# Optimization experiments

Hardware: AMD Instinct MI355X
Metric: run time of the kernel (lower is better)

## Reference

```python
import jax, jax.numpy as jnp
import numpy as np

B = 8
RESOLUTIONS = [65, 129, 257, 513, 1025]
NUM_POINTS = [0, 4096, 16384, 65536, 262144]
CLIP_MIN = -1e9
FINAL = 1025          # last resolution (both axes)
B_MIN, B_MAX = -1.0, 1.0
BALANCE = 0.5


def setup_inputs() -> dict:
    key = jax.random.key(0)
    k1, k2, k3, k4 = jax.random.split(key, 4)
    return {
        "w1": jax.random.normal(k1, (2, 256), jnp.float32),
        "b1": jax.random.normal(k2, (256,), jnp.float32),
        "w2": jax.random.normal(k3, (256, 1), jnp.float32),
        "b2": jax.random.normal(k4, (1,), jnp.float32),
    }


def _interp_bilinear_ac(x, H, W):
    """F.interpolate(..., mode='bilinear', align_corners=True). x: [B, C, h, w]."""
    b, c, h, w = x.shape
    ys = jnp.linspace(0.0, h - 1.0, H)
    xs = jnp.linspace(0.0, w - 1.0, W)
    y0 = jnp.floor(ys).astype(jnp.int32)
    y1 = jnp.minimum(y0 + 1, h - 1)
    wy = ys - y0
    x0 = jnp.floor(xs).astype(jnp.int32)
    x1 = jnp.minimum(x0 + 1, w - 1)
    wx = xs - x0
    # interpolate rows, then columns
    top = x[:, :, y0, :] * (1.0 - wy)[None, None, :, None] + x[:, :, y1, :] * wy[None, None, :, None]
    return top[:, :, :, x0] * (1.0 - wx) + top[:, :, :, x1] * wx


def _batch_eval(coords, w1, b1, w2, b2):
    """coords: [B, N, 2] in final-resolution pixel space (align_corners=False mapping).
    Returns occupancy [B, N] (C == 1)."""
    coords2d = coords / FINAL + 0.5 / FINAL                 # normalize to [0, 1]
    p = coords2d * (B_MAX - B_MIN) + B_MIN                  # [B, N, 2] in world coords
    h = jax.nn.relu(jnp.einsum('bnd,dh->bnh', p, w1) + b1)  # [B, N, 256]
    occ = jax.nn.sigmoid(jnp.einsum('bnh,ho->bno', h, w2) + b2)
    return occ[..., 0]


def reference(w1, b1, w2, b2):
    occ = None
    for i, res in enumerate(RESOLUTIONS):
        if i == 0:
            # init_coords: grid of res x res points spanning [0, FINAL-1]
            xs = jnp.linspace(0.0, FINAL - 1.0, res)
            gy, gx = jnp.meshgrid(xs, xs, indexing='ij')          # y rows, x cols
            coords = jnp.stack([gx.ravel(), gy.ravel()], axis=-1)  # [N, 2] (x, y)
            coords = jnp.broadcast_to(coords, (B, res * res, 2))
            o = _batch_eval(coords, w1, b1, w2, b2)               # [B, N]
            occ = o.reshape(B, 1, res, res)                       # [B, C, H, W]
        else:
            occ = _interp_bilinear_ac(occ, res, res)
            npt = NUM_POINTS[i]
            if npt <= 0:
                continue
            # uncertainty = -|occ - balance_value|
            unc = -jnp.abs(occ - BALANCE)                          # [B, 1, H, W]
            flat_unc = unc.reshape(B, res * res)
            scores, idx = jax.lax.top_k(flat_unc, npt)             # [B, npt]
            px = (idx % res).astype(jnp.float32)
            py = (idx // res).astype(jnp.float32)
            stride = (FINAL - 1.0) / (res - 1.0)
            coords = jnp.stack([px, py], axis=-1) * stride         # [B, npt, 2]
            new_vals = _batch_eval(coords, w1, b1, w2, b2)         # [B, npt]
            occ_flat = occ.reshape(B, res * res)
            old_vals = jnp.take_along_axis(occ_flat, idx, axis=1)
            vals = jnp.where(scores >= CLIP_MIN, new_vals, old_vals)
            occ_flat = jax.vmap(lambda o, i2, v: o.at[i2].set(v))(occ_flat, idx, vals)
            occ = occ_flat.reshape(B, 1, res, res)
    return occ
```

## Files before the change

kernel.cpp:

```cpp
#include <hip/hip_runtime.h>
#include <stdint.h>

#define HID 256
#define NMAXPIX (1025 * 1025)
#define NREP 4
#define NSEG 2048
#define SELMAX 2112
#define FLAG31 0x80000000u

#define HA_OFF   0
#define HB_OFF   8192
#define HC_OFF   16384
#define SCAL_OFF 20480
#define BLKT_OFF 20544
#define STAGE_U32 21120

#define ALOAD32(p)  __hip_atomic_load((p), __ATOMIC_RELAXED, __HIP_MEMORY_SCOPE_AGENT)
#define ASTORE32(p, v) __hip_atomic_store((p), (v), __ATOMIC_RELAXED, __HIP_MEMORY_SCOPE_AGENT)

__device__ __forceinline__ float mlp_eval4(float wx, float wy,
                                           const float4* __restrict__ w1x,
                                           const float4* __restrict__ w1y,
                                           const float4* __restrict__ vb1,
                                           const float4* __restrict__ vw2, float b2v) {
    const float C0 = (float)(0.5 / 1025.0);
    float px = (wx / 1025.0f + C0) * 2.0f - 1.0f;
    float py = (wy / 1025.0f + C0) * 2.0f - 1.0f;
    float a0 = 0.f, a1 = 0.f, a2 = 0.f, a3 = 0.f;
#pragma unroll 8
    for (int q = 0; q < HID / 4; ++q) {
        float4 a = w1x[q], b = w1y[q], c = vb1[q], d = vw2[q];
        float h0 = px * a.x + py * b.x + c.x;
        float h1 = px * a.y + py * b.y + c.y;
        float h2 = px * a.z + py * b.z + c.z;
        float h3 = px * a.w + py * b.w + c.w;
        h0 = h0 > 0.f ? h0 : 0.f;
        h1 = h1 > 0.f ? h1 : 0.f;
        h2 = h2 > 0.f ? h2 : 0.f;
        h3 = h3 > 0.f ? h3 : 0.f;
        a0 += h0 * d.x;
        a1 += h1 * d.y;
        a2 += h2 * d.z;
        a3 += h3 * d.w;
    }
    float x = ((a0 + a1) + (a2 + a3)) + b2v;
    float r;
    if (x >= 0.f) { r = 1.0f / (1.0f + expf(-x)); }
    else { float e = expf(x); r = e / (1.0f + e); }
    return r;
}

__device__ __forceinline__ uint32_t block_exscan_256(uint32_t v, volatile uint32_t* lds4) {
    int lane = threadIdx.x & 63, w = threadIdx.x >> 6;
    uint32_t inc = v;
#pragma unroll
    for (int d = 1; d < 64; d <<= 1) {
        uint32_t o = (uint32_t)__shfl_up((int)inc, d, 64);
        if (lane >= d) inc += o;
    }
    if (lane == 63) lds4[w] = inc;
    __syncthreads();
    uint32_t woff = 0;
    for (int i = 0; i < w; ++i) woff += lds4[i];
    return woff + inc - v;
}

__device__ void scan_dev(const uint32_t* __restrict__ hist, int NB,
                         uint32_t rem_in, uint32_t prefix_in, int shift,
                         uint32_t* outp, uint32_t* outr,
                         volatile uint32_t* lds4, volatile uint32_t* ldspair) {
    int tid = threadIdx.x;
    int C = NB >> 8;
    int b0 = NB - (tid + 1) * C;
    uint32_t cnts[8];
#pragma unroll
    for (int k = 0; k < 8; ++k) cnts[k] = 0;
    for (int rep = 0; rep < NREP; ++rep) {
        const uint4* p = (const uint4*)(hist + (size_t)rep * NB + b0);
#pragma unroll
        for (int g = 0; g < 2; ++g) {
            if (g * 4 < C) {
                uint4 v = p[g];
                cnts[g * 4 + 0] += v.x;
                cnts[g * 4 + 1] += v.y;
                cnts[g * 4 + 2] += v.z;
                cnts[g * 4 + 3] += v.w;
            }
        }
    }
    uint32_t ssum = 0;
    for (int k = 0; k < C; ++k) ssum += cnts[k];
    uint32_t excl = block_exscan_256(ssum, lds4);
    uint32_t run = excl;
    for (int k = 0; k < C; ++k) {
        uint32_t c = cnts[C - 1 - k];
        if (rem_in > run && rem_in <= run + c) {
            ldspair[0] = (prefix_in << shift) | (uint32_t)(b0 + C - 1 - k);
            ldspair[1] = rem_in - run;
        }
        run += c;
    }
    __syncthreads();
    *outp = ldspair[0];
    *outr = ldspair[1];
}

__global__ __launch_bounds__(256) void k_eval0z(const float* __restrict__ w1, const float* __restrict__ b1,
                                                const float* __restrict__ w2, const float* __restrict__ b2,
                                                float* __restrict__ occ, uint32_t* __restrict__ zbuf, int zcount) {
    __shared__ alignas(16) float sw1[2 * HID];
    __shared__ alignas(16) float sb1[HID];
    __shared__ alignas(16) float sw2[HID];
    int tid = threadIdx.x;
    for (int i = tid; i < 2 * HID; i += 256) sw1[i] = w1[i];
    sb1[tid] = b1[tid];
    sw2[tid] = w2[tid];
    __syncthreads();
    int gtid = blockIdx.x * 256 + tid;
    int nthreads = gridDim.x * 256;
    for (int i = gtid; i < zcount; i += nthreads) zbuf[i] = 0;
    for (int n = gtid; n < 65 * 65; n += nthreads) {
        int i = n / 65, j = n % 65;
        occ[n] = mlp_eval4(16.0f * (float)j, 16.0f * (float)i,
                           (const float4*)sw1, (const float4*)(sw1 + HID),
                           (const float4*)sb1, (const float4*)sw2, b2[0]);
    }
}

__global__ __launch_bounds__(256) void k_upkey(const float* __restrict__ in, int rp,
                                               float* __restrict__ outg, int r, int nb, int bstride,
                                               uint32_t* __restrict__ keys,
                                               uint32_t* __restrict__ histA) {
    __shared__ uint32_t hist[2048];
    int tid = threadIdx.x;
    for (int k = tid; k < 2048; k += 256) hist[k] = 0;
    __syncthreads();
    int N = r * r;
    int lane = tid & 63;
    int gstride = gridDim.x * 256;
    for (int n0 = blockIdx.x * 256; n0 < N; n0 += gstride) {
        int n = n0 + tid;
        bool act = n < N;
        uint32_t key = 0;
        if (act) {
            int i = n / r, j = n % r;
            int i2 = i >> 1, j2 = j >> 1;
            float v;
            if ((i & 1) == 0) {
                if ((j & 1) == 0) {
                    v = in[i2 * rp + j2];
                } else {
                    float a = in[i2 * rp + j2], b = in[i2 * rp + j2 + 1];
                    v = a * 0.5f + b * 0.5f;
                }
            } else {
                if ((j & 1) == 0) {
                    float a = in[i2 * rp + j2], b = in[(i2 + 1) * rp + j2];
                    v = a * 0.5f + b * 0.5f;
                } else {
                    float a = in[i2 * rp + j2],      c = in[i2 * rp + j2 + 1];
                    float b = in[(i2 + 1) * rp + j2], d = in[(i2 + 1) * rp + j2 + 1];
                    float t1 = a * 0.5f + b * 0.5f;
                    float t2 = c * 0.5f + d * 0.5f;
                    v = t1 * 0.5f + t2 * 0.5f;
                }
            }
            for (int k = 0; k < nb; ++k) outg[(size_t)k * bstride + n] = v;
            float unc = -fabsf(v - 0.5f);
            uint32_t u = __float_as_uint(unc);
            key = (u & 0x80000000u) ? ~u : (u | 0x80000000u);
            keys[n] = key;
        }
        uint32_t bin = key >> 21;
        unsigned long long m = __ballot(act);
        if (m) {
            int leader = __ffsll(m) - 1;
            uint32_t lbin = (uint32_t)__shfl((int)bin, leader, 64);
            unsigned long long smk = __ballot(act && bin == lbin);
            if (smk == m) {
                if (lane == leader) atomicAdd(&hist[lbin], (uint32_t)__popcll(m));
            } else if (act) {
                atomicAdd(&hist[bin], 1u);
            }
        }
    }
    __syncthreads();
    uint32_t* myrep = histA + (size_t)(blockIdx.x & (NREP - 1)) * 2048;
    for (int k = tid; k < 2048; k += 256) {
        uint32_t c = hist[k];
        if (c) atomicAdd(&myrep[k], c);
    }
}

__global__ __launch_bounds__(256) void k_histmid(const uint32_t* __restrict__ keys, int N,
                                                 const uint32_t* __restrict__ prevHist,
                                                 uint32_t* __restrict__ scal,
                                                 int useNpt, uint32_t npt, int scalInIdx, int shift,
                                                 int scalOutIdx,
                                                 int fshift, int bshift, uint32_t bmask,
                                                 uint32_t* __restrict__ outHist, int NBout) {
    __shared__ uint32_t lh[2048];
    __shared__ uint32_t lds4[4];
    __shared__ uint32_t ldspair[2];
    int tid = threadIdx.x, lane = tid & 63;
    uint32_t rem_in = useNpt ? npt : scal[scalInIdx + 1];
    uint32_t pfx_in = useNpt ? 0u  : scal[scalInIdx];
    uint32_t pfx, rem;
    scan_dev(prevHist, 2048, rem_in, pfx_in, shift, &pfx, &rem, lds4, ldspair);
    if (blockIdx.x == 0 && tid == 0) { scal[scalOutIdx] = pfx; scal[scalOutIdx + 1] = rem; }
    for (int k = tid; k < 2048; k += 256) lh[k] = 0;
    __syncthreads();
    int gstride = gridDim.x * 256;
    for (int base = blockIdx.x * 256; base < N; base += gstride) {
        int n = base + tid;
        bool inb = n < N;
        uint32_t key = inb ? keys[n] : 0u;
        bool flt = inb && ((key >> fshift) == pfx);
        uint32_t bin = (key >> bshift) & bmask;
        unsigned long long m = __ballot(flt);
        if (m) {
            int leader = __ffsll(m) - 1;
            uint32_t lbin = (uint32_t)__shfl((int)bin, leader, 64);
            unsigned long long smk = __ballot(flt && bin == lbin);
            if (smk == m) {
                if (lane == leader) atomicAdd(&lh[lbin], (uint32_t)__popcll(m));
            } else if (flt) {
                atomicAdd(&lh[bin], 1u);
            }
        }
    }
    __syncthreads();
    uint32_t* myrep = outHist + (size_t)(blockIdx.x & (NREP - 1)) * NBout;
    for (int k = tid; k < NBout; k += 256) {
        uint32_t c = lh[k];
        if (c) atomicAdd(&myrep[k], c);
    }
}

__global__ __launch_bounds__(256, 2) void k_seleval(const uint32_t* __restrict__ keys, int N, int seglen,
                                                    const uint32_t* __restrict__ histC,
                                                    const uint32_t* __restrict__ scal,
                                                    uint32_t* __restrict__ blkT,
                                                    int r, float stride,
                                                    float* __restrict__ occ, int nb, int bstride,
                                                    const float* __restrict__ w1, const float* __restrict__ b1,
                                                    const float* __restrict__ w2, const float* __restrict__ b2) {
    __shared__ alignas(16) float sw1[2 * HID];
    __shared__ alignas(16) float sb1[HID];
    __shared__ alignas(16) float sw2[HID];
    __shared__ uint32_t lds4[4];
    __shared__ uint32_t ldspair[2];
    __shared__ uint32_t wcnt[4];
    __shared__ uint32_t bp_s;
    __shared__ uint32_t selcnt;
    __shared__ uint32_t selidx[SELMAX];
    int tid = threadIdx.x, lane = tid & 63, w = tid >> 6;
    int blk = blockIdx.x;
    for (int i = tid; i < 2 * HID; i += 256) sw1[i] = w1[i];
    sb1[tid] = b1[tid];
    sw2[tid] = w2[tid];
    if (tid == 0) selcnt = 0;
    __syncthreads();

    uint32_t K, t;
    scan_dev(histC, 1024, scal[3], scal[2], 10, &K, &t, lds4, ldspair);

    int wv = blk * 4 + w;
    int s0 = wv * seglen;
    int s1 = s0 + seglen; if (s1 > N) s1 = N;
    {
        uint32_t tcnt = 0;
        for (int base = s0; base < s1; base += 64) {
            int n = base + lane;
            if (n < s1) tcnt += (keys[n] == K) ? 1u : 0u;
        }
#pragma unroll
        for (int d = 32; d; d >>= 1) tcnt += (uint32_t)__shfl_down((int)tcnt, d, 64);
        if (lane == 0) wcnt[w] = tcnt;
    }
    __syncthreads();
    if (w == 0) {
        if (lane == 0) {
            uint32_t tot = wcnt[0] + wcnt[1] + wcnt[2] + wcnt[3];
            ASTORE32(&blkT[blk], tot | FLAG31);
        }
        uint32_t bp = 0;
        for (int i = lane; i < blk; i += 64) {
            uint32_t v;
            for (;;) {
                v = ALOAD32(&blkT[i]);
                if (v & FLAG31) break;
                __builtin_amdgcn_s_sleep(2);
            }
            bp += v & 0x7FFFFFFFu;
        }
#pragma unroll
        for (int d = 32; d; d >>= 1) bp += (uint32_t)__shfl_down((int)bp, d, 64);
        if (lane == 0) bp_s = bp;
    }
    __syncthreads();
    uint32_t tp = bp_s;
    for (int ww = 0; ww < w; ++ww) tp += wcnt[ww];

    uint32_t tie_run = tp;
    unsigned long long lowmask = (lane == 63) ? ~0ull >> 1 : ((1ull << lane) - 1ull);
    for (int base = s0; base < s1; base += 64) {
        int n = base + lane;
        bool inb = n < s1;
        uint32_t key = inb ? keys[n] : 0u;
        bool gt = inb && (key > K);
        bool tie = inb && (key == K);
        unsigned long long tm = __ballot(tie);
        uint32_t trank = tie_run + (uint32_t)__popcll(tm & lowmask);
        bool sel = gt || (tie && trank < t);
        unsigned long long smk = __ballot(sel);
        if (smk) {
            int leader = __ffsll(smk) - 1;
            uint32_t wbase = 0;
            if (lane == leader) wbase = atomicAdd(&selcnt, (uint32_t)__popcll(smk));
            wbase = (uint32_t)__shfl((int)wbase, leader, 64);
            if (sel) selidx[wbase + (uint32_t)__popcll(smk & lowmask)] = (uint32_t)n;
        }
        tie_run += (uint32_t)__popcll(tm);
    }
    __syncthreads();

    uint32_t cnt = selcnt;
    float vb2 = b2[0];
    const float4* w1x = (const float4*)sw1;
    const float4* w1y = (const float4*)(sw1 + HID);
    const float4* vb1 = (const float4*)sb1;
    const float4* vw2 = (const float4*)sw2;
    const float C0 = (float)(0.5 / 1025.0);
    for (uint32_t bb = 0; bb < cnt; bb += 1024) {
        uint32_t i0 = bb + tid, i1 = i0 + 256, i2 = i0 + 512, i3 = i0 + 768;
        bool v0 = i0 < cnt, v1 = i1 < cnt, v2 = i2 < cnt, v3 = i3 < cnt;
        int nA = v0 ? (int)selidx[i0] : 0;
        int nB = v1 ? (int)selidx[i1] : 0;
        int nC = v2 ? (int)selidx[i2] : 0;
        int nD = v3 ? (int)selidx[i3] : 0;
        int iA = nA / r, jA = nA % r;
        int iB = nB / r, jB = nB % r;
        int iC = nC / r, jC = nC % r;
        int iD = nD / r, jD = nD % r;
        float px0 = ((stride * (float)jA) / 1025.0f + C0) * 2.0f - 1.0f;
        float py0 = ((stride * (float)iA) / 1025.0f + C0) * 2.0f - 1.0f;
        float px1 = ((stride * (float)jB) / 1025.0f + C0) * 2.0f - 1.0f;
        float py1 = ((stride * (float)iB) / 1025.0f + C0) * 2.0f - 1.0f;
        float px2 = ((stride * (float)jC) / 1025.0f + C0) * 2.0f - 1.0f;
        float py2 = ((stride * (float)iC) / 1025.0f + C0) * 2.0f - 1.0f;
        float px3 = ((stride * (float)jD) / 1025.0f + C0) * 2.0f - 1.0f;
        float py3 = ((stride * (float)iD) / 1025.0f + C0) * 2.0f - 1.0f;
        float4 A0 = {0, 0, 0, 0}, A1 = {0, 0, 0, 0}, A2 = {0, 0, 0, 0}, A3 = {0, 0, 0, 0};
#pragma unroll 4
        for (int q = 0; q < HID / 4; ++q) {
            float4 a = w1x[q], b = w1y[q], c = vb1[q], d = vw2[q];
#define STEP(P, AX) {                                              \
            float h0 = px##P * a.x + py##P * b.x + c.x;            \
            float h1 = px##P * a.y + py##P * b.y + c.y;            \
            float h2 = px##P * a.z + py##P * b.z + c.z;            \
            float h3 = px##P * a.w + py##P * b.w + c.w;            \
            h0 = h0 > 0.f ? h0 : 0.f;                              \
            h1 = h1 > 0.f ? h1 : 0.f;                              \
            h2 = h2 > 0.f ? h2 : 0.f;                              \
            h3 = h3 > 0.f ? h3 : 0.f;                              \
            AX.x += h0 * d.x; AX.y += h1 * d.y;                    \
            AX.z += h2 * d.z; AX.w += h3 * d.w; }
            STEP(0, A0) STEP(1, A1) STEP(2, A2) STEP(3, A3)
#undef STEP
        }
#define FIN(VQ, AX, NP) if (VQ) {                                  \
        float x = ((AX.x + AX.y) + (AX.z + AX.w)) + vb2;           \
        float rr;                                                  \
        if (x >= 0.f) { rr = 1.0f / (1.0f + expf(-x)); }           \
        else { float e = expf(x); rr = e / (1.0f + e); }           \
        for (int k = 0; k < nb; ++k) occ[(size_t)k * bstride + NP] = rr; }
        FIN(v0, A0, nA) FIN(v1, A1, nB) FIN(v2, A2, nC) FIN(v3, A3, nD)
#undef FIN
    }
}

__global__ __launch_bounds__(256) void k_bcast(const float* __restrict__ src, float* __restrict__ dst, int N) {
    int q = blockIdx.x * 256 + threadIdx.x;
    int n = q * 4;
    if (n + 3 < N) {
        float4 v = *(const float4*)(src + n);
#pragma unroll
        for (int k = 0; k < 8; ++k) *(float4*)(dst + (size_t)k * N + n) = v;
    } else if (n < N) {
        for (int m = n; m < N; ++m) {
            float v = src[m];
#pragma unroll
            for (int k = 0; k < 8; ++k) dst[(size_t)k * N + m] = v;
        }
    }
}

extern "C" void kernel_launch(void* const* d_in, const int* in_sizes, int n_in,
                              void* d_out, int out_size, void* d_ws, size_t ws_size,
                              hipStream_t stream) {
    const float* w1 = (const float*)d_in[0];
    const float* b1 = (const float*)d_in[1];
    const float* w2 = (const float*)d_in[2];
    const float* b2 = (const float*)d_in[3];
    float* out = (float*)d_out;

    const size_t A = (((size_t)NMAXPIX * 4) + 255) & ~(size_t)255;
    const size_t SMALL_BYTES = (size_t)4 * STAGE_U32 * 4;
    const size_t need = 3 * A + SMALL_BYTES;

    int fused8 = (ws_size >= need);
    char* base = fused8 ? (char*)d_ws : (char*)d_out;
    float* buf0 = (float*)(base);
    float* buf1 = (float*)(base + A);
    uint32_t* keys = (uint32_t*)(base + 2 * A);
    uint32_t* smallb = (uint32_t*)(base + 3 * A);

    k_eval0z<<<dim3(512), dim3(256), 0, stream>>>(w1, b1, w2, b2, buf0, smallb, 4 * STAGE_U32);

    const int resA[5] = {65, 129, 257, 513, 1025};
    const int nptA[5] = {0, 4096, 16384, 65536, 262144};
    float* cur = buf0;
    float* nxt = buf1;
    for (int s = 1; s < 5; ++s) {
        int rp = resA[s - 1], r = resA[s];
        int N = r * r;
        uint32_t npt = (uint32_t)nptA[s];
        uint32_t* sm = smallb + (size_t)(s - 1) * STAGE_U32;
        uint32_t* histA = sm + HA_OFF;
        uint32_t* histB = sm + HB_OFF;
        uint32_t* histC = sm + HC_OFF;
        uint32_t* scal  = sm + SCAL_OFF;
        uint32_t* blkT  = sm + BLKT_OFF;
        int nb1 = (N + 255) / 256;
        int nbu = nb1 < 1024 ? nb1 : 1024;
        int seglen = (N + NSEG - 1) / NSEG;
        float stride = 1024.0f / (float)(r - 1);

        int last = (s == 4);
        float* stage_out = (last && fused8) ? out : nxt;
        int nb = (last && fused8) ? 8 : 1;
        int bstride = (last && fused8) ? NMAXPIX : 0;

        k_upkey<<<dim3(nbu), dim3(256), 0, stream>>>(cur, rp, stage_out, r, nb, bstride, keys, histA);
        k_histmid<<<dim3(512), dim3(256), 0, stream>>>(keys, N, histA, scal, 1, npt, 0, 0,
                                                       0, 21, 10, 0x7FFu, histB, 2048);
        k_histmid<<<dim3(512), dim3(256), 0, stream>>>(keys, N, histB, scal, 0, 0u, 0, 11,
                                                       2, 10, 0, 0x3FFu, histC, 1024);
        k_seleval<<<dim3(NSEG / 4), dim3(256), 0, stream>>>(keys, N, seglen, histC, scal, blkT,
                                                            r, stride, stage_out, nb, bstride,
                                                            w1, b1, w2, b2);
        if (!(last && fused8)) { float* tmp = cur; cur = nxt; nxt = tmp; }
    }
    if (!fused8) {
        k_bcast<<<dim3(((NMAXPIX + 3) / 4 + 255) / 256), dim3(256), 0, stream>>>(cur, out, NMAXPIX);
    }
}
```

Measured before the change: 257.8 us.

## Use single-block select kernels for small stages and split tie-count from selection

The first two refinement stages (129 and 257 resolution) now run in one 1024-thread block that does the upsample, a three-pass radix select in LDS and ordered compaction. A separate kernel then evaluates the MLP on the selected points, four points per thread. For the larger stages, the decoupled look-back spin on per-block tie counts is replaced by a separate k_segcnt kernel that writes per-wave tie counts, which k_seleval then prefix-sums. NREP is doubled to 8. Together this removes several launches and inter-block spin waits for the small stages, at the cost of an extra launch and an extra read of the keys for the large stages.

```diff
diff --git a/kernel.cpp b/kernel.cpp
--- a/kernel.cpp
+++ b/kernel.cpp
@@ -3,20 +3,16 @@
 
 #define HID 256
 #define NMAXPIX (1025 * 1025)
-#define NREP 4
+#define NREP 8
 #define NSEG 2048
 #define SELMAX 2112
-#define FLAG31 0x80000000u
-
-#define HA_OFF   0
-#define HB_OFF   8192
-#define HC_OFF   16384
-#define SCAL_OFF 20480
-#define BLKT_OFF 20544
-#define STAGE_U32 21120
-
-#define ALOAD32(p)  __hip_atomic_load((p), __ATOMIC_RELAXED, __HIP_MEMORY_SCOPE_AGENT)
-#define ASTORE32(p, v) __hip_atomic_store((p), (v), __ATOMIC_RELAXED, __HIP_MEMORY_SCOPE_AGENT)
+
+#define HISTA_OFF 0
+#define HISTB_OFF 16384
+#define HISTC_OFF 32768
+#define SCAL_OFF  40960
+#define TIC_OFF   41024
+#define STAGE_U32 43072
 
 __device__ __forceinline__ float mlp_eval4(float wx, float wy,
                                            const float4* __restrict__ w1x,
@@ -50,6 +46,38 @@
     return r;
 }
 
+__device__ __forceinline__ float upsample_val(const float* __restrict__ in, int rp, int r, int n) {
+    int i = n / r, j = n % r;
+    int i2 = i >> 1, j2 = j >> 1;
+    float v;
+    if ((i & 1) == 0) {
+        if ((j & 1) == 0) {
+            v = in[i2 * rp + j2];
+        } else {
+            float a = in[i2 * rp + j2], b = in[i2 * rp + j2 + 1];
+            v = a * 0.5f + b * 0.5f;
+        }
+    } else {
+        if ((j & 1) == 0) {
+            float a = in[i2 * rp + j2], b = in[(i2 + 1) * rp + j2];
+            v = a * 0.5f + b * 0.5f;
+        } else {
+            float a = in[i2 * rp + j2],      c = in[i2 * rp + j2 + 1];
+            float b = in[(i2 + 1) * rp + j2], d = in[(i2 + 1) * rp + j2 + 1];
+            float t1 = a * 0.5f + b * 0.5f;
+            float t2 = c * 0.5f + d * 0.5f;
+            v = t1 * 0.5f + t2 * 0.5f;
+        }
+    }
+    return v;
+}
+
+__device__ __forceinline__ uint32_t key_of(float v) {
+    float unc = -fabsf(v - 0.5f);
+    uint32_t u = __float_as_uint(unc);
+    return (u & 0x80000000u) ? ~u : (u | 0x80000000u);
+}
+
 __device__ __forceinline__ uint32_t block_exscan_256(uint32_t v, volatile uint32_t* lds4) {
     int lane = threadIdx.x & 63, w = threadIdx.x >> 6;
     uint32_t inc = v;
@@ -62,6 +90,21 @@
     __syncthreads();
     uint32_t woff = 0;
     for (int i = 0; i < w; ++i) woff += lds4[i];
+    return woff + inc - v;
+}
+
+__device__ __forceinline__ uint32_t block_exscan_1024(uint32_t v, volatile uint32_t* lds16) {
+    int lane = threadIdx.x & 63, w = threadIdx.x >> 6;
+    uint32_t inc = v;
+#pragma unroll
+    for (int d = 1; d < 64; d <<= 1) {
+        uint32_t o = (uint32_t)__shfl_up((int)inc, d, 64);
+        if (lane >= d) inc += o;
+    }
+    if (lane == 63) lds16[w] = inc;
+    __syncthreads();
+    uint32_t woff = 0;
+    for (int i = 0; i < w; ++i) woff += lds16[i];
     return woff + inc - v;
 }
 
@@ -103,6 +146,48 @@
     __syncthreads();
     *outp = ldspair[0];
     *outr = ldspair[1];
+}
+
+__device__ void scan_lds(const uint32_t* hist, int NB,
+                         uint32_t rem_in, uint32_t prefix_in, int shift,
+                         uint32_t* outp, uint32_t* outr,
+                         volatile uint32_t* lds16, volatile uint32_t* ldspair) {
+    int tid = threadIdx.x;
+    int C = NB >> 10;
+    int b0 = NB - (tid + 1) * C;
+    uint32_t c0 = hist[b0];
+    uint32_t c1 = (C == 2) ? hist[b0 + 1] : 0u;
+    uint32_t ssum = c0 + c1;
+    uint32_t excl = block_exscan_1024(ssum, lds16);
+    uint32_t run = excl;
+    if (C == 2) {
+        if (rem_in > run && rem_in <= run + c1) {
+            ldspair[0] = (prefix_in << shift) | (uint32_t)(b0 + 1);
+            ldspair[1] = rem_in - run;
+        }
+        run += c1;
+    }
+    if (rem_in > run && rem_in <= run + c0) {
+        ldspair[0] = (prefix_in << shift) | (uint32_t)b0;
+        ldspair[1] = rem_in - run;
+    }
+    __syncthreads();
+    *outp = ldspair[0];
+    *outr = ldspair[1];
+}
+
+__device__ __forceinline__ void lds_hist_add(uint32_t* hist, bool act, uint32_t bin, int lane) {
+    unsigned long long m = __ballot(act);
+    if (m) {
+        int leader = __ffsll(m) - 1;
+        uint32_t lbin = (uint32_t)__shfl((int)bin, leader, 64);
+        unsigned long long smk = __ballot(act && bin == lbin);
+        if (smk == m) {
+            if (lane == leader) atomicAdd(&hist[lbin], (uint32_t)__popcll(m));
+        } else if (act) {
+            atomicAdd(&hist[bin], 1u);
+        }
+    }
 }
 
 __global__ __launch_bounds__(256) void k_eval0z(const float* __restrict__ w1, const float* __restrict__ b1,
@@ -127,6 +212,176 @@
     }
 }
 
+__global__ __launch_bounds__(1024) void k_small(const float* __restrict__ in, int rp,
+                                                float* __restrict__ outg, int r, uint32_t npt,
+                                                uint32_t* __restrict__ keys,
+                                                uint32_t* __restrict__ list) {
+    __shared__ uint32_t hist[2048];
+    __shared__ uint32_t lds16[16];
+    __shared__ uint32_t ldspair[2];
+    __shared__ uint32_t iterw[16], itert[16];
+    int tid = threadIdx.x, lane = tid & 63, w = tid >> 6;
+    int N = r * r;
+    for (int k = tid; k < 2048; k += 1024) hist[k] = 0;
+    __syncthreads();
+
+    for (int n0 = 0; n0 < N; n0 += 1024) {
+        int n = n0 + tid;
+        bool act = n < N;
+        uint32_t key = 0;
+        if (act) {
+            float v = upsample_val(in, rp, r, n);
+            outg[n] = v;
+            key = key_of(v);
+            keys[n] = key;
+        }
+        lds_hist_add(hist, act, key >> 21, lane);
+    }
+    __syncthreads();
+    uint32_t pfx, rem;
+    scan_lds(hist, 2048, npt, 0u, 0, &pfx, &rem, lds16, ldspair);
+    __syncthreads();
+
+    for (int k = tid; k < 2048; k += 1024) hist[k] = 0;
+    __syncthreads();
+    for (int n0 = 0; n0 < N; n0 += 1024) {
+        int n = n0 + tid;
+        bool inb = n < N;
+        uint32_t key = inb ? keys[n] : 0u;
+        bool flt = inb && ((key >> 21) == pfx);
+        lds_hist_add(hist, flt, (key >> 10) & 0x7FFu, lane);
+    }
+    __syncthreads();
+    scan_lds(hist, 2048, rem, pfx, 11, &pfx, &rem, lds16, ldspair);
+    __syncthreads();
+
+    for (int k = tid; k < 1024; k += 1024) hist[k] = 0;
+    __syncthreads();
+    for (int n0 = 0; n0 < N; n0 += 1024) {
+        int n = n0 + tid;
+        bool inb = n < N;
+        uint32_t key = inb ? keys[n] : 0u;
+        bool flt = inb && ((key >> 10) == pfx);
+        lds_hist_add(hist, flt, key & 0x3FFu, lane);
+    }
+    __syncthreads();
+    uint32_t K, t;
+    scan_lds(hist, 1024, rem, pfx, 10, &K, &t, lds16, ldspair);
+    __syncthreads();
+
+    unsigned long long lowmask = (lane == 63) ? ~0ull >> 1 : ((1ull << lane) - 1ull);
+    uint32_t running_sel = 0, running_tie = 0;
+    for (int base = 0; base < N; base += 4096) {
+        int nb0 = base + w * 256;
+        uint32_t kq[4];
+        unsigned long long tmq[4], smq[4];
+        uint32_t wtie = 0;
+#pragma unroll
+        for (int q = 0; q < 4; ++q) {
+            int n = nb0 + q * 64 + lane;
+            bool inb = n < N;
+            kq[q] = inb ? keys[n] : 0u;
+            bool tie = inb && (kq[q] == K);
+            tmq[q] = __ballot(tie);
+            wtie += (uint32_t)__popcll(tmq[q]);
+        }
+        if (lane == 0) itert[w] = wtie;
+        __syncthreads();
+        uint32_t wtp = running_tie;
+        for (int ww = 0; ww < w; ++ww) wtp += itert[ww];
+        uint32_t wsel = 0;
+#pragma unroll
+        for (int q = 0; q < 4; ++q) {
+            int n = nb0 + q * 64 + lane;
+            bool inb = n < N;
+            bool gt = inb && (kq[q] > K);
+            bool tie = inb && (kq[q] == K);
+            uint32_t trank = wtp + (uint32_t)__popcll(tmq[q] & lowmask);
+            bool sel = gt || (tie && trank < t);
+            smq[q] = __ballot(sel);
+            wtp += (uint32_t)__popcll(tmq[q]);
+            wsel += (uint32_t)__popcll(smq[q]);
+        }
+        if (lane == 0) iterw[w] = wsel;
+        __syncthreads();
+        uint32_t wsp = running_sel;
+        for (int ww = 0; ww < w; ++ww) wsp += iterw[ww];
+#pragma unroll
+        for (int q = 0; q < 4; ++q) {
+            int n = nb0 + q * 64 + lane;
+            bool sel = (smq[q] >> lane) & 1ull;
+            if (sel) list[wsp + (uint32_t)__popcll(smq[q] & lowmask)] = (uint32_t)n;
+            wsp += (uint32_t)__popcll(smq[q]);
+        }
+        for (int ww = 0; ww < 16; ++ww) { running_sel += iterw[ww]; running_tie += itert[ww]; }
+        __syncthreads();
+    }
+}
+
+__global__ __launch_bounds__(256) void k_evalpts(const uint32_t* __restrict__ outlist, int r, float stride,
+                                                 float* __restrict__ occ,
+                                                 const float* __restrict__ w1, const float* __restrict__ b1,
+                                                 const float* __restrict__ w2, const float* __restrict__ b2) {
+    __shared__ alignas(16) float sw1[2 * HID];
+    __shared__ alignas(16) float sb1[HID];
+    __shared__ alignas(16) float sw2[HID];
+    int tid = threadIdx.x;
+    for (int i = tid; i < 2 * HID; i += 256) sw1[i] = w1[i];
+    sb1[tid] = b1[tid];
+    sw2[tid] = w2[tid];
+    __syncthreads();
+    const float4* w1x = (const float4*)sw1;
+    const float4* w1y = (const float4*)(sw1 + HID);
+    const float4* vb1 = (const float4*)sb1;
+    const float4* vw2 = (const float4*)sw2;
+    float vb2 = b2[0];
+    const float C0 = (float)(0.5 / 1025.0);
+    int gid = blockIdx.x * 256 + tid;
+    uint4 nn = ((const uint4*)outlist)[gid];
+    uint32_t n0 = nn.x, n1 = nn.y, n2 = nn.z, n3 = nn.w;
+    float px0, py0, px1, py1, px2, py2, px3, py3;
+    {
+        int i0 = (int)n0 / r, j0 = (int)n0 % r;
+        int i1 = (int)n1 / r, j1 = (int)n1 % r;
+        int i2 = (int)n2 / r, j2 = (int)n2 % r;
+        int i3 = (int)n3 / r, j3 = (int)n3 % r;
+        px0 = ((stride * (float)j0) / 1025.0f + C0) * 2.0f - 1.0f;
+        py0 = ((stride * (float)i0) / 1025.0f + C0) * 2.0f - 1.0f;
+        px1 = ((stride * (float)j1) / 1025.0f + C0) * 2.0f - 1.0f;
+        py1 = ((stride * (float)i1) / 1025.0f + C0) * 2.0f - 1.0f;
+        px2 = ((stride * (float)j2) / 1025.0f + C0) * 2.0f - 1.0f;
+        py2 = ((stride * (float)i2) / 1025.0f + C0) * 2.0f - 1.0f;
+        px3 = ((stride * (float)j3) / 1025.0f + C0) * 2.0f - 1.0f;
+        py3 = ((stride * (float)i3) / 1025.0f + C0) * 2.0f - 1.0f;
+    }
+    float4 A0 = {0, 0, 0, 0}, A1 = {0, 0, 0, 0}, A2 = {0, 0, 0, 0}, A3 = {0, 0, 0, 0};
+#pragma unroll 4
+    for (int q = 0; q < HID / 4; ++q) {
+        float4 a = w1x[q], b = w1y[q], c = vb1[q], d = vw2[q];
+#define STEP(P, AX) {                                              \
+        float h0 = px##P * a.x + py##P * b.x + c.x;                \
+        float h1 = px##P * a.y + py##P * b.y + c.y;                \
+        float h2 = px##P * a.z + py##P * b.z + c.z;                \
+        float h3 = px##P * a.w + py##P * b.w + c.w;                \
+        h0 = h0 > 0.f ? h0 : 0.f;                                  \
+        h1 = h1 > 0.f ? h1 : 0.f;                                  \
+        h2 = h2 > 0.f ? h2 : 0.f;                                  \
+        h3 = h3 > 0.f ? h3 : 0.f;                                  \
+        AX.x += h0 * d.x; AX.y += h1 * d.y;                        \
+        AX.z += h2 * d.z; AX.w += h3 * d.w; }
+        STEP(0, A0) STEP(1, A1) STEP(2, A2) STEP(3, A3)
+#undef STEP
+    }
+#define FIN(AX, NP) {                                              \
+        float x = ((AX.x + AX.y) + (AX.z + AX.w)) + vb2;           \
+        float rr;                                                  \
+        if (x >= 0.f) { rr = 1.0f / (1.0f + expf(-x)); }           \
+        else { float e = expf(x); rr = e / (1.0f + e); }           \
+        occ[NP] = rr; }
+    FIN(A0, n0) FIN(A1, n1) FIN(A2, n2) FIN(A3, n3)
+#undef FIN
+}
+
 __global__ __launch_bounds__(256) void k_upkey(const float* __restrict__ in, int rp,
                                                float* __restrict__ outg, int r, int nb, int bstride,
                                                uint32_t* __restrict__ keys,
@@ -143,46 +398,12 @@
         bool act = n < N;
         uint32_t key = 0;
         if (act) {
-            int i = n / r, j = n % r;
-            int i2 = i >> 1, j2 = j >> 1;
-            float v;
-            if ((i & 1) == 0) {
-                if ((j & 1) == 0) {
-                    v = in[i2 * rp + j2];
-                } else {
-                    float a = in[i2 * rp + j2], b = in[i2 * rp + j2 + 1];
-                    v = a * 0.5f + b * 0.5f;
-                }
-            } else {
-                if ((j & 1) == 0) {
-                    float a = in[i2 * rp + j2], b = in[(i2 + 1) * rp + j2];
-                    v = a * 0.5f + b * 0.5f;
-                } else {
-                    float a = in[i2 * rp + j2],      c = in[i2 * rp + j2 + 1];
-                    float b = in[(i2 + 1) * rp + j2], d = in[(i2 + 1) * rp + j2 + 1];
-                    float t1 = a * 0.5f + b * 0.5f;
-                    float t2 = c * 0.5f + d * 0.5f;
-                    v = t1 * 0.5f + t2 * 0.5f;
-                }
-            }
+            float v = upsample_val(in, rp, r, n);
             for (int k = 0; k < nb; ++k) outg[(size_t)k * bstride + n] = v;
-            float unc = -fabsf(v - 0.5f);
-            uint32_t u = __float_as_uint(unc);
-            key = (u & 0x80000000u) ? ~u : (u | 0x80000000u);
+            key = key_of(v);
             keys[n] = key;
         }
-        uint32_t bin = key >> 21;
-        unsigned long long m = __ballot(act);
-        if (m) {
-            int leader = __ffsll(m) - 1;
-            uint32_t lbin = (uint32_t)__shfl((int)bin, leader, 64);
-            unsigned long long smk = __ballot(act && bin == lbin);
-            if (smk == m) {
-                if (lane == leader) atomicAdd(&hist[lbin], (uint32_t)__popcll(m));
-            } else if (act) {
-                atomicAdd(&hist[bin], 1u);
-            }
-        }
+        lds_hist_add(hist, act, key >> 21, lane);
     }
     __syncthreads();
     uint32_t* myrep = histA + (size_t)(blockIdx.x & (NREP - 1)) * 2048;
@@ -216,18 +437,7 @@
         bool inb = n < N;
         uint32_t key = inb ? keys[n] : 0u;
         bool flt = inb && ((key >> fshift) == pfx);
-        uint32_t bin = (key >> bshift) & bmask;
-        unsigned long long m = __ballot(flt);
-        if (m) {
-            int leader = __ffsll(m) - 1;
-            uint32_t lbin = (uint32_t)__shfl((int)bin, leader, 64);
-            unsigned long long smk = __ballot(flt && bin == lbin);
-            if (smk == m) {
-                if (lane == leader) atomicAdd(&lh[lbin], (uint32_t)__popcll(m));
-            } else if (flt) {
-                atomicAdd(&lh[bin], 1u);
-            }
-        }
+        lds_hist_add(lh, flt, (key >> bshift) & bmask, lane);
     }
     __syncthreads();
     uint32_t* myrep = outHist + (size_t)(blockIdx.x & (NREP - 1)) * NBout;
@@ -237,72 +447,60 @@
     }
 }
 
-__global__ __launch_bounds__(256, 2) void k_seleval(const uint32_t* __restrict__ keys, int N, int seglen,
-                                                    const uint32_t* __restrict__ histC,
-                                                    const uint32_t* __restrict__ scal,
-                                                    uint32_t* __restrict__ blkT,
-                                                    int r, float stride,
-                                                    float* __restrict__ occ, int nb, int bstride,
-                                                    const float* __restrict__ w1, const float* __restrict__ b1,
-                                                    const float* __restrict__ w2, const float* __restrict__ b2) {
+__global__ __launch_bounds__(256) void k_segcnt(const uint32_t* __restrict__ keys, int N, int seglen,
+                                                const uint32_t* __restrict__ histC,
+                                                uint32_t* __restrict__ scal,
+                                                uint32_t* __restrict__ tic) {
+    __shared__ uint32_t lds4[4];
+    __shared__ uint32_t ldspair[2];
+    int tid = threadIdx.x, lane = tid & 63;
+    uint32_t rem2 = scal[3], pfx2 = scal[2];
+    uint32_t K, t;
+    scan_dev(histC, 1024, rem2, pfx2, 10, &K, &t, lds4, ldspair);
+    if (blockIdx.x == 0 && tid == 0) { scal[4] = K; scal[5] = t; }
+    int wv = blockIdx.x * 4 + (tid >> 6);
+    int s0 = wv * seglen;
+    int s1 = s0 + seglen; if (s1 > N) s1 = N;
+    uint32_t tcnt = 0;
+    for (int base = s0; base < s1; base += 64) {
+        int n = base + lane;
+        if (n < s1) tcnt += (keys[n] == K) ? 1u : 0u;
+    }
+#pragma unroll
+    for (int d = 32; d; d >>= 1) tcnt += (uint32_t)__shfl_down((int)tcnt, d, 64);
+    if (lane == 0) tic[wv] = tcnt;
+}
+
+__global__ __launch_bounds__(256) void k_seleval(const uint32_t* __restrict__ keys, int N, int seglen,
+                                                 const uint32_t* __restrict__ scal,
+                                                 const uint32_t* __restrict__ tic,
+                                                 int r, float stride,
+                                                 float* __restrict__ occ, int nb, int bstride,
+                                                 const float* __restrict__ w1, const float* __restrict__ b1,
+                                                 const float* __restrict__ w2, const float* __restrict__ b2) {
     __shared__ alignas(16) float sw1[2 * HID];
     __shared__ alignas(16) float sb1[HID];
     __shared__ alignas(16) float sw2[HID];
-    __shared__ uint32_t lds4[4];
-    __shared__ uint32_t ldspair[2];
-    __shared__ uint32_t wcnt[4];
-    __shared__ uint32_t bp_s;
     __shared__ uint32_t selcnt;
     __shared__ uint32_t selidx[SELMAX];
-    int tid = threadIdx.x, lane = tid & 63, w = tid >> 6;
-    int blk = blockIdx.x;
+    int tid = threadIdx.x, lane = tid & 63;
     for (int i = tid; i < 2 * HID; i += 256) sw1[i] = w1[i];
     sb1[tid] = b1[tid];
     sw2[tid] = w2[tid];
     if (tid == 0) selcnt = 0;
     __syncthreads();
-
-    uint32_t K, t;
-    scan_dev(histC, 1024, scal[3], scal[2], 10, &K, &t, lds4, ldspair);
-
-    int wv = blk * 4 + w;
+    uint32_t K = scal[4], t = scal[5];
+
+    int wv = blockIdx.x * 4 + (tid >> 6);
+    uint32_t tp = 0;
+    for (int i = lane; i < wv; i += 64) tp += tic[i];
+#pragma unroll
+    for (int d = 32; d; d >>= 1) tp += (uint32_t)__shfl_down((int)tp, d, 64);
+    tp = (uint32_t)__shfl((int)tp, 0, 64);
+
+    uint32_t tie_run = tp;
     int s0 = wv * seglen;
     int s1 = s0 + seglen; if (s1 > N) s1 = N;
-    {
-        uint32_t tcnt = 0;
-        for (int base = s0; base < s1; base += 64) {
-            int n = base + lane;
-            if (n < s1) tcnt += (keys[n] == K) ? 1u : 0u;
-        }
-#pragma unroll
-        for (int d = 32; d; d >>= 1) tcnt += (uint32_t)__shfl_down((int)tcnt, d, 64);
-        if (lane == 0) wcnt[w] = tcnt;
-    }
-    __syncthreads();
-    if (w == 0) {
-        if (lane == 0) {
-            uint32_t tot = wcnt[0] + wcnt[1] + wcnt[2] + wcnt[3];
-            ASTORE32(&blkT[blk], tot | FLAG31);
-        }
-        uint32_t bp = 0;
-        for (int i = lane; i < blk; i += 64) {
-            uint32_t v;
-            for (;;) {
-                v = ALOAD32(&blkT[i]);
-                if (v & FLAG31) break;
-                __builtin_amdgcn_s_sleep(2);
-            }
-            bp += v & 0x7FFFFFFFu;
-        }
-#pragma unroll
-        for (int d = 32; d; d >>= 1) bp += (uint32_t)__shfl_down((int)bp, d, 64);
-        if (lane == 0) bp_s = bp;
-    }
-    __syncthreads();
-    uint32_t tp = bp_s;
-    for (int ww = 0; ww < w; ++ww) tp += wcnt[ww];
-
-    uint32_t tie_run = tp;
     unsigned long long lowmask = (lane == 63) ? ~0ull >> 1 : ((1ull << lane) - 1ull);
     for (int base = s0; base < s1; base += 64) {
         int n = base + lane;
@@ -407,7 +605,8 @@
 
     const size_t A = (((size_t)NMAXPIX * 4) + 255) & ~(size_t)255;
     const size_t SMALL_BYTES = (size_t)4 * STAGE_U32 * 4;
-    const size_t need = 3 * A + SMALL_BYTES;
+    const size_t LIST_BYTES = (size_t)16384 * 4;
+    const size_t need = 3 * A + SMALL_BYTES + LIST_BYTES;
 
     int fused8 = (ws_size >= need);
     char* base = fused8 ? (char*)d_ws : (char*)d_out;
@@ -415,23 +614,30 @@
     float* buf1 = (float*)(base + A);
     uint32_t* keys = (uint32_t*)(base + 2 * A);
     uint32_t* smallb = (uint32_t*)(base + 3 * A);
+    uint32_t* list = (uint32_t*)(base + 3 * A + SMALL_BYTES);
 
     k_eval0z<<<dim3(512), dim3(256), 0, stream>>>(w1, b1, w2, b2, buf0, smallb, 4 * STAGE_U32);
+
+    k_small<<<dim3(1), dim3(1024), 0, stream>>>(buf0, 65, buf1, 129, 4096u, keys, list);
+    k_evalpts<<<dim3(4), dim3(256), 0, stream>>>(list, 129, 1024.0f / 128.0f, buf1, w1, b1, w2, b2);
+
+    k_small<<<dim3(1), dim3(1024), 0, stream>>>(buf1, 129, buf0, 257, 16384u, keys, list);
+    k_evalpts<<<dim3(16), dim3(256), 0, stream>>>(list, 257, 1024.0f / 256.0f, buf0, w1, b1, w2, b2);
 
     const int resA[5] = {65, 129, 257, 513, 1025};
     const int nptA[5] = {0, 4096, 16384, 65536, 262144};
     float* cur = buf0;
     float* nxt = buf1;
-    for (int s = 1; s < 5; ++s) {
+    for (int s = 3; s < 5; ++s) {
         int rp = resA[s - 1], r = resA[s];
         int N = r * r;
         uint32_t npt = (uint32_t)nptA[s];
         uint32_t* sm = smallb + (size_t)(s - 1) * STAGE_U32;
-        uint32_t* histA = sm + HA_OFF;
-        uint32_t* histB = sm + HB_OFF;
-        uint32_t* histC = sm + HC_OFF;
+        uint32_t* histA = sm + HISTA_OFF;
+        uint32_t* histB = sm + HISTB_OFF;
+        uint32_t* histC = sm + HISTC_OFF;
         uint32_t* scal  = sm + SCAL_OFF;
-        uint32_t* blkT  = sm + BLKT_OFF;
+        uint32_t* tic   = sm + TIC_OFF;
         int nb1 = (N + 255) / 256;
         int nbu = nb1 < 1024 ? nb1 : 1024;
         int seglen = (N + NSEG - 1) / NSEG;
@@ -447,9 +653,9 @@
                                                        0, 21, 10, 0x7FFu, histB, 2048);
         k_histmid<<<dim3(512), dim3(256), 0, stream>>>(keys, N, histB, scal, 0, 0u, 0, 11,
                                                        2, 10, 0, 0x3FFu, histC, 1024);
-        k_seleval<<<dim3(NSEG / 4), dim3(256), 0, stream>>>(keys, N, seglen, histC, scal, blkT,
-                                                            r, stride, stage_out, nb, bstride,
-                                                            w1, b1, w2, b2);
+        k_segcnt<<<dim3(NSEG / 4), dim3(256), 0, stream>>>(keys, N, seglen, histC, scal, tic);
+        k_seleval<<<dim3(NSEG / 4), dim3(256), 0, stream>>>(keys, N, seglen, scal, tic, r, stride,
+                                                            stage_out, nb, bstride, w1, b1, w2, b2);
         if (!(last && fused8)) { float* tmp = cur; cur = nxt; nxt = tmp; }
     }
     if (!fused8) {
```

Result: slower. 370.7 us (+43.8%).
